# Kernel optimization log

Measured on AMD Instinct MI355X. Metric: run time of the kernel, lower is better.

Reference implementation:

```python
import jax, jax.numpy as jnp
import numpy as np

D = 1024          # dim_in == dim_out
H = 16            # num_heads
G = 4             # num_kv_groups
HD = D // H       # head_dim = 64
GS = H // G       # group_size = 4
S = 2048          # context_length / seq_len
B = 2
EPS = 1e-05


def setup_inputs() -> dict:
    key = jax.random.key(0)
    ks = jax.random.split(key, 12)
    sd = 0.02
    return {
        "x":  jax.random.normal(ks[0], (B, S, D), jnp.float32),
        # torch.nn.Linear weights are stored [out_features, in_features]
        "wq": jax.random.normal(ks[1], (D, D), jnp.float32) * sd,
        "wk": jax.random.normal(ks[2], (G * HD, D), jnp.float32) * sd,
        "wv": jax.random.normal(ks[3], (G * HD, D), jnp.float32) * sd,
        "wo": jax.random.normal(ks[4], (D, D), jnp.float32) * sd,
        "w1": jax.random.normal(ks[5], (4 * D, D), jnp.float32) * sd,
        "w2": jax.random.normal(ks[6], (D, 4 * D), jnp.float32) * sd,
        "g1": jnp.ones((D,), jnp.float32),
        "b1": jnp.zeros((D,), jnp.float32),
        "g2": jnp.ones((D,), jnp.float32),
        "b2": jnp.zeros((D,), jnp.float32),
    }


def _layernorm(x, gamma, beta):
    mean = jnp.mean(x, axis=-1, keepdims=True)
    var = jnp.var(x, axis=-1, keepdims=True)  # unbiased=False
    return (x - mean) * jax.lax.rsqrt(var + EPS) * gamma + beta


def _gelu_tanh(x):
    c = jnp.sqrt(jnp.asarray(2.0 / jnp.pi, x.dtype))
    return 0.5 * x * (1.0 + jnp.tanh(c * (x + 0.044715 * x ** 3)))


def _gqa(x, wq, wk, wv, wo):
    b, s, _ = x.shape
    q = (x @ wq.T).reshape(b, s, H, HD).transpose(0, 2, 1, 3)   # [B,H,S,hd]
    k = (x @ wk.T).reshape(b, s, G, HD).transpose(0, 2, 1, 3)   # [B,G,S,hd]
    v = (x @ wv.T).reshape(b, s, G, HD).transpose(0, 2, 1, 3)
    k = jnp.repeat(k, GS, axis=1)                               # [B,H,S,hd]
    v = jnp.repeat(v, GS, axis=1)
    scores = jnp.einsum('bhqd,bhkd->bhqk', q, k)                # [B,H,S,S]
    causal = jnp.tril(jnp.ones((s, s), bool))
    scores = jnp.where(causal, scores, -jnp.inf)
    attn = jax.nn.softmax(scores / jnp.sqrt(jnp.asarray(HD, scores.dtype)), axis=-1)
    ctx = jnp.einsum('bhqk,bhkd->bhqd', attn, v)                # [B,H,S,hd]
    ctx = ctx.transpose(0, 2, 1, 3).reshape(b, s, D)
    return ctx @ wo.T


def reference(x, wq, wk, wv, wo, w1, w2, g1, b1, g2, b2):
    h = x + _gqa(_layernorm(x, g1, b1), wq, wk, wv, wo)
    ff = _layernorm(h, g2, b2) @ w1.T
    ff = _gelu_tanh(ff) @ w2.T
    return h + ff
```

## Files before the change

kernel.cpp:

```cpp
#include <hip/hip_runtime.h>
#include <stdint.h>

typedef __bf16 bf16_t;
typedef bf16_t bf16x8 __attribute__((ext_vector_type(8)));
typedef bf16_t bf16x4 __attribute__((ext_vector_type(4)));
typedef float f32x4 __attribute__((ext_vector_type(4)));

#define DEVFN static __device__ __forceinline__

DEVFN void gload_lds16(const void* g, void* l) {
  __builtin_amdgcn_global_load_lds((const __attribute__((address_space(1))) void*)g,
                                   (__attribute__((address_space(3))) void*)l, 16, 0, 0);
}

DEVFN float gelu_f(float x) {
  float u = 0.7978845608028654f * (x + 0.044715f * x * x * x);
  float e = __expf(2.0f * u);
  float t = 1.0f - 2.0f / (e + 1.0f);
  return 0.5f * x * (1.0f + t);
}

template <int CTRL>
DEVFN float dpp_rot(float x) {
  int i = __builtin_bit_cast(int, x);
  int r = __builtin_amdgcn_update_dpp(i, i, CTRL, 0xF, 0xF, false);
  return __builtin_bit_cast(float, r);
}
DEVFN float dpp_sum16(float x) {
  x += dpp_rot<0x121>(x);
  x += dpp_rot<0x122>(x);
  x += dpp_rot<0x124>(x);
  x += dpp_rot<0x128>(x);
  return x;
}

__global__ void cvt_kernel(const float* __restrict__ s, bf16_t* __restrict__ d, int n4) {
  int i = blockIdx.x * blockDim.x + threadIdx.x;
  int stride = gridDim.x * blockDim.x;
  for (; i < n4; i += stride) {
    float4 v = ((const float4*)s)[i];
    bf16x4 o;
    o[0] = (bf16_t)v.x; o[1] = (bf16_t)v.y; o[2] = (bf16_t)v.z; o[3] = (bf16_t)v.w;
    ((bf16x4*)d)[i] = o;
  }
}

__global__ void cvt4_kernel(const float* __restrict__ wq, const float* __restrict__ wk,
                            const float* __restrict__ wv, const float* __restrict__ wo,
                            bf16_t* __restrict__ qkv_dst, bf16_t* __restrict__ wo_dst) {
  int i = blockIdx.x * blockDim.x + threadIdx.x;
  int stride = gridDim.x * blockDim.x;
  for (; i < 655360; i += stride) {
    const float* s;
    bf16_t* d;
    int j;
    if (i < 262144) { s = wq; d = qkv_dst; j = i; }
    else if (i < 327680) { s = wk; d = qkv_dst + 1048576; j = i - 262144; }
    else if (i < 393216) { s = wv; d = qkv_dst + 1310720; j = i - 327680; }
    else { s = wo; d = wo_dst; j = i - 393216; }
    float4 v = ((const float4*)s)[j];
    bf16x4 o;
    o[0] = (bf16_t)v.x; o[1] = (bf16_t)v.y; o[2] = (bf16_t)v.z; o[3] = (bf16_t)v.w;
    ((bf16x4*)d)[j] = o;
  }
}

__global__ __launch_bounds__(256) void ln_kernel(const float* __restrict__ in,
                                                 const float* __restrict__ gamma,
                                                 const float* __restrict__ beta,
                                                 bf16_t* __restrict__ out) {
  const int row = blockIdx.x;
  const int tid = threadIdx.x;
  const float4 v = ((const float4*)(in + (size_t)row * 1024))[tid];
  float s = v.x + v.y + v.z + v.w;
  float q = v.x * v.x + v.y * v.y + v.z * v.z + v.w * v.w;
#pragma unroll
  for (int off = 1; off < 64; off <<= 1) {
    s += __shfl_xor(s, off);
    q += __shfl_xor(q, off);
  }
  __shared__ float ss[4], qs[4];
  if ((tid & 63) == 0) { ss[tid >> 6] = s; qs[tid >> 6] = q; }
  __syncthreads();
  s = ss[0] + ss[1] + ss[2] + ss[3];
  q = qs[0] + qs[1] + qs[2] + qs[3];
  const float mean = s * (1.0f / 1024.0f);
  const float var = q * (1.0f / 1024.0f) - mean * mean;
  const float rstd = rsqrtf(var + 1e-5f);
  const float4 g4 = ((const float4*)gamma)[tid];
  const float4 b4 = ((const float4*)beta)[tid];
  bf16x4 o;
  o[0] = (bf16_t)((v.x - mean) * rstd * g4.x + b4.x);
  o[1] = (bf16_t)((v.y - mean) * rstd * g4.y + b4.y);
  o[2] = (bf16_t)((v.z - mean) * rstd * g4.z + b4.z);
  o[3] = (bf16_t)((v.w - mean) * rstd * g4.w + b4.w);
  *(bf16x4*)(out + (size_t)row * 1024 + tid * 4) = o;
}

template <int EPI>
__global__ __launch_bounds__(256, 3)
void gemm_bt(const bf16_t* __restrict__ A, const bf16_t* __restrict__ W,
             bf16_t* outb, float* outf, const float* resid, int M, int N, int K) {
  __shared__ __align__(16) bf16_t As[4][64 * 32];
  __shared__ __align__(16) bf16_t Bs[4][128 * 32];
  const int tid = threadIdx.x;
  const int lane = tid & 63;
  const int wid = tid >> 6;
  const int l15 = lane & 15;
  const int l4 = lane >> 4;

  const int nwg = gridDim.x * gridDim.y;
  const int bid = blockIdx.y * gridDim.x + blockIdx.x;
  const int cpx = nwg >> 3;
  const int swz = (bid & 7) * cpx + (bid >> 3);
  const int m0 = (swz / gridDim.x) * 64;
  const int n0 = (swz % gridDim.x) * 128;

  const int wr = wid >> 1;
  const int wc = wid & 1;

  const int sr = lane >> 2;
  const int sk = (lane & 3) * 8;
  const bf16_t* aBase = A + (size_t)(m0 + wid * 16 + sr) * K + sk;
  const bf16_t* bBase = W + (size_t)(n0 + wid * 32 + sr) * K + sk;
  const size_t rowOff16 = (size_t)16 * K;

  f32x4 acc[2][4] = {};
  const int NT = K / 32;

  auto stage = [&](int buf, int t) {
    const int ko = t * 32;
    gload_lds16(aBase + ko, &As[buf][wid * 512]);
    gload_lds16(bBase + ko, &Bs[buf][wid * 1024]);
    gload_lds16(bBase + ko + rowOff16, &Bs[buf][wid * 1024 + 512]);
  };

  stage(0, 0);
  if (NT > 1) stage(1, 1);
  if (NT > 2) stage(2, 2);

  for (int t = 0; t < NT; ++t) {
    if (t + 2 < NT)      __builtin_amdgcn_s_waitcnt(0xF76);
    else if (t + 1 < NT) __builtin_amdgcn_s_waitcnt(0xF73);
    else                 __builtin_amdgcn_s_waitcnt(0xF70);
    __builtin_amdgcn_s_barrier();
    __builtin_amdgcn_sched_barrier(0);
    if (t + 3 < NT) stage((t + 3) & 3, t + 3);
    const int buf = t & 3;
    bf16x8 af[2], bfr[4];
#pragma unroll
    for (int i = 0; i < 2; ++i)
      af[i] = *(const bf16x8*)&As[buf][(wr * 32 + i * 16 + l15) * 32 + l4 * 8];
#pragma unroll
    for (int j = 0; j < 4; ++j)
      bfr[j] = *(const bf16x8*)&Bs[buf][(wc * 64 + j * 16 + l15) * 32 + l4 * 8];
#pragma unroll
    for (int i = 0; i < 2; ++i)
#pragma unroll
      for (int j = 0; j < 4; ++j)
        acc[i][j] = __builtin_amdgcn_mfma_f32_16x16x32_bf16(af[i], bfr[j], acc[i][j], 0, 0, 0);
  }

  const int col0 = n0 + wc * 64 + l15;
  const int row0 = m0 + wr * 32 + l4 * 4;
#pragma unroll
  for (int i = 0; i < 2; ++i) {
#pragma unroll
    for (int r = 0; r < 4; ++r) {
      const size_t row = (size_t)(row0 + i * 16 + r);
#pragma unroll
      for (int j = 0; j < 4; ++j) {
        const size_t idx = row * N + col0 + j * 16;
        const float v = acc[i][j][r];
        if constexpr (EPI == 0) {
          outb[idx] = (bf16_t)v;
        } else if constexpr (EPI == 1) {
          outb[idx] = (bf16_t)gelu_f(v);
        } else {
          outf[idx] = resid[idx] + v;
        }
      }
    }
  }
}

static __device__ const int kQbTab[40] = {0,1,2,3,4,4,5,5,6,6,7,7,8,8,8,9,9,9,10,10,10,
                                          11,11,11,12,12,12,12,13,13,13,13,14,14,14,14,15,15,15,15};
static __device__ const int kCTab[40]  = {0,0,0,0,0,1,0,1,0,1,0,1,0,1,2,0,1,2,0,1,2,
                                          0,1,2,0,1,2,3,0,1,2,3,0,1,2,3,0,1,2,3};
static __device__ const int kPrefix16[16] = {0,1,2,3,4,6,8,10,12,15,18,21,24,28,32,36};

__global__ __launch_bounds__(256, 3) void attn_kernel(const bf16_t* __restrict__ qkv,
                                                      bf16_t* __restrict__ pO,
                                                      float* __restrict__ pML) {
  __shared__ __align__(16) bf16_t Ks[2][64 * 68];
  __shared__ __align__(16) bf16_t Vt[2][64 * 68];
  __shared__ __align__(16) bf16_t Ps[4][32 * 68];
  const int tid = threadIdx.x, lane = tid & 63, wid = tid >> 6;
  const int l15 = lane & 15, l4 = lane >> 4;
  const int bx = blockIdx.x;
  const int qb = kQbTab[bx] * 128;
  const int kv_lo = kCTab[bx] * 512;
  const int kv_hi = min(qb + 128, kv_lo + 512);
  const int h = blockIdx.y, b = blockIdx.z;
  const int g = h >> 2;
  const int slot = (b * 16 + h) * 40 + bx;
  const size_t RS = 1536;
  const bf16_t* qbase = qkv + (size_t)b * 2048 * RS + h * 64;
  const bf16_t* kbase = qkv + (size_t)b * 2048 * RS + 1024 + g * 64;
  const bf16_t* vbase = kbase + 256;
  const float C2S = 0.125f * 1.44269504088896340736f;

  bf16x8 qf[2][2];
#pragma unroll
  for (int rf = 0; rf < 2; ++rf)
#pragma unroll
    for (int kc = 0; kc < 2; ++kc) {
      bf16x8 raw = *(const bf16x8*)(qbase + (size_t)(qb + wid * 32 + rf * 16 + l15) * RS +
                                    kc * 32 + l4 * 8);
#pragma unroll
      for (int e = 0; e < 8; ++e) qf[rf][kc][e] = (bf16_t)((float)raw[e] * C2S);
    }

  f32x4 po[2][4] = {};
  float l_i[2][4] = {};

  const int sKrow = tid >> 2, sKc = (tid & 3) * 16;
  const int sVkey = tid & 63, sVd = (tid >> 6) * 16;
  const bf16_t* kRowPtr = kbase + (size_t)sKrow * RS + sKc;
  const bf16_t* vRowPtr = vbase + (size_t)sVkey * RS + sVd;

  uint4 k0 = *(const uint4*)(kRowPtr + (size_t)kv_lo * RS);
  uint4 k1 = *(const uint4*)(kRowPtr + (size_t)kv_lo * RS + 8);
  bf16x8 v0 = *(const bf16x8*)(vRowPtr + (size_t)kv_lo * RS);
  bf16x8 v1 = *(const bf16x8*)(vRowPtr + (size_t)kv_lo * RS + 8);
  *(uint4*)&Ks[0][sKrow * 68 + sKc] = k0;
  *(uint4*)&Ks[0][sKrow * 68 + sKc + 8] = k1;
#pragma unroll
  for (int i = 0; i < 8; ++i) {
    Vt[0][(sVd + i) * 68 + sVkey] = v0[i];
    Vt[0][(sVd + 8 + i) * 68 + sVkey] = v1[i];
  }

  const int fb0 = qb + wid * 32;
  int cur = 0;
  for (int kv0 = kv_lo; kv0 < kv_hi; kv0 += 64) {
    __syncthreads();
    const bool more = (kv0 + 64) < kv_hi;
    if (more) {
      const bf16_t* kp = kRowPtr + (size_t)(kv0 + 64) * RS;
      const bf16_t* vp = vRowPtr + (size_t)(kv0 + 64) * RS;
      k0 = *(const uint4*)kp;
      k1 = *(const uint4*)(kp + 8);
      v0 = *(const bf16x8*)vp;
      v1 = *(const bf16x8*)(vp + 8);
    }

    f32x4 sAcc[2][4] = {};
#pragma unroll
    for (int jt = 0; jt < 4; ++jt) {
#pragma unroll
      for (int kc = 0; kc < 2; ++kc) {
        bf16x8 kf = *(const bf16x8*)&Ks[cur][(jt * 16 + l15) * 68 + kc * 32 + l4 * 8];
        sAcc[0][jt] = __builtin_amdgcn_mfma_f32_16x16x32_bf16(qf[0][kc], kf, sAcc[0][jt], 0, 0, 0);
        sAcc[1][jt] = __builtin_amdgcn_mfma_f32_16x16x32_bf16(qf[1][kc], kf, sAcc[1][jt], 0, 0, 0);
      }
    }

#pragma unroll
    for (int rf = 0; rf < 2; ++rf) {
      const int fb = fb0 + rf * 16;
      if (kv0 > fb + 15) continue;
      bf16_t* psb = &Ps[wid][(rf * 16 + l4 * 4) * 68 + l15];
      float rsum[4] = {0.f, 0.f, 0.f, 0.f};
      const bool diag = (kv0 + 63 > fb);
#pragma unroll
      for (int jt = 0; jt < 4; ++jt)
#pragma unroll
        for (int r = 0; r < 4; ++r) {
          float sv = sAcc[rf][jt][r];
          if (diag) {
            const int key = kv0 + jt * 16 + l15;
            sv = (key <= fb + l4 * 4 + r) ? sv : -3.0e38f;
          }
          const float e = exp2f(sv);
          rsum[r] += e;
          psb[r * 68 + jt * 16] = (bf16_t)e;
        }
#pragma unroll
      for (int r = 0; r < 4; ++r) l_i[rf][r] += dpp_sum16(rsum[r]);
    }

    if (kv0 <= fb0 + 31) {
      const bool do0 = (kv0 <= fb0 + 15);
#pragma unroll
      for (int kc = 0; kc < 2; ++kc) {
        bf16x8 pa1 = *(const bf16x8*)&Ps[wid][(16 + l15) * 68 + kc * 32 + l4 * 8];
        bf16x8 pa0;
        if (do0) pa0 = *(const bf16x8*)&Ps[wid][l15 * 68 + kc * 32 + l4 * 8];
#pragma unroll
        for (int jd = 0; jd < 4; ++jd) {
          bf16x8 vf = *(const bf16x8*)&Vt[cur][(jd * 16 + l15) * 68 + kc * 32 + l4 * 8];
          if (do0) po[0][jd] = __builtin_amdgcn_mfma_f32_16x16x32_bf16(pa0, vf, po[0][jd], 0, 0, 0);
          po[1][jd] = __builtin_amdgcn_mfma_f32_16x16x32_bf16(pa1, vf, po[1][jd], 0, 0, 0);
        }
      }
    }

    if (more) {
      *(uint4*)&Ks[cur ^ 1][sKrow * 68 + sKc] = k0;
      *(uint4*)&Ks[cur ^ 1][sKrow * 68 + sKc + 8] = k1;
#pragma unroll
      for (int i = 0; i < 8; ++i) {
        Vt[cur ^ 1][(sVd + i) * 68 + sVkey] = v0[i];
        Vt[cur ^ 1][(sVd + 8 + i) * 68 + sVkey] = v1[i];
      }
    }
    cur ^= 1;
  }

#pragma unroll
  for (int rf = 0; rf < 2; ++rf) {
#pragma unroll
    for (int r = 0; r < 4; ++r) {
      const int lrow = wid * 32 + rf * 16 + l4 * 4 + r;
      if (l15 == 0) {
        pML[((size_t)slot * 128 + lrow) * 2] = 0.0f;
        pML[((size_t)slot * 128 + lrow) * 2 + 1] = l_i[rf][r];
      }
#pragma unroll
      for (int jd = 0; jd < 4; ++jd)
        pO[((size_t)slot * 128 + lrow) * 64 + jd * 16 + l15] = (bf16_t)po[rf][jd][r];
    }
  }
}

__global__ __launch_bounds__(256) void attn_combine(const bf16_t* __restrict__ pO,
                                                    const float* __restrict__ pML,
                                                    bf16_t* __restrict__ ctx) {
  const int i = blockIdx.x, h = blockIdx.y, b = blockIdx.z;
  const int C = (i >> 2) + 1;
  const int base = (b * 16 + h) * 40 + kPrefix16[i];
  const int row = threadIdx.x >> 1;
  const int half = (threadIdx.x & 1) * 32;
  float m = -3.0e38f;
  for (int c = 0; c < C; ++c)
    m = fmaxf(m, pML[((size_t)(base + c) * 128 + row) * 2]);
  float L = 0.0f, acc[32];
#pragma unroll
  for (int e = 0; e < 32; ++e) acc[e] = 0.0f;
  for (int c = 0; c < C; ++c) {
    const float mc = pML[((size_t)(base + c) * 128 + row) * 2];
    const float lc = pML[((size_t)(base + c) * 128 + row) * 2 + 1];
    const float w = exp2f(mc - m);
    L += w * lc;
    const bf16_t* op = pO + ((size_t)(base + c) * 128 + row) * 64 + half;
#pragma unroll
    for (int j = 0; j < 4; ++j) {
      bf16x8 v = *(const bf16x8*)(op + j * 8);
#pragma unroll
      for (int e = 0; e < 8; ++e) acc[j * 8 + e] += w * (float)v[e];
    }
  }
  const float inv = 1.0f / L;
  bf16_t* outp = ctx + ((size_t)b * 2048 + i * 128 + row) * 1024 + h * 64 + half;
#pragma unroll
  for (int j = 0; j < 4; ++j) {
    bf16x8 o;
#pragma unroll
    for (int e = 0; e < 8; ++e) o[e] = (bf16_t)(acc[j * 8 + e] * inv);
    *(bf16x8*)(outp + j * 8) = o;
  }
}

extern "C" void kernel_launch(void* const* d_in, const int* in_sizes, int n_in,
                              void* d_out, int out_size, void* d_ws, size_t ws_size,
                              hipStream_t stream) {
  const float* x = (const float*)d_in[0];
  const float* wq = (const float*)d_in[1];
  const float* wk = (const float*)d_in[2];
  const float* wv = (const float*)d_in[3];
  const float* wo = (const float*)d_in[4];
  const float* w1 = (const float*)d_in[5];
  const float* w2 = (const float*)d_in[6];
  const float* g1 = (const float*)d_in[7];
  const float* b1 = (const float*)d_in[8];
  const float* g2 = (const float*)d_in[9];
  const float* b2 = (const float*)d_in[10];
  float* out = (float*)d_out;

  char* ws = (char*)d_ws;
  bf16_t* qkv = (bf16_t*)(ws + 0);
  bf16_t* ctx = (bf16_t*)(ws + 12582912);
  bf16_t* wo_b = (bf16_t*)(ws + 20971520);
  bf16_t* wqkv_b = (bf16_t*)(ws + 23068672);
  bf16_t* h1 = (bf16_t*)(ws + 26214400);
  bf16_t* pO = (bf16_t*)(ws + 23068672);
  float* pML = (float*)(ws + 45088768);
  bf16_t* w1_b = (bf16_t*)(ws + 0);
  bf16_t* w2_b = (bf16_t*)(ws + 8388608);
  bf16_t* h2 = (bf16_t*)(ws + 16777216);
  bf16_t* ff = (bf16_t*)(ws + 25165824);

  auto cvt = [&](const float* s, bf16_t* d, int n) {
    int n4 = n / 4;
    int grid = (n4 + 255) / 256;
    if (grid > 2048) grid = 2048;
    cvt_kernel<<<grid, 256, 0, stream>>>(s, d, n4);
  };
  cvt4_kernel<<<2048, 256, 0, stream>>>(wq, wk, wv, wo, wqkv_b, wo_b);

  ln_kernel<<<4096, 256, 0, stream>>>(x, g1, b1, h1);
  gemm_bt<0><<<dim3(12, 64), 256, 0, stream>>>(h1, wqkv_b, qkv, nullptr, nullptr, 4096, 1536, 1024);
  attn_kernel<<<dim3(40, 16, 2), 256, 0, stream>>>(qkv, pO, pML);
  cvt(w1, w1_b, 4194304);
  attn_combine<<<dim3(16, 16, 2), 256, 0, stream>>>(pO, pML, ctx);
  gemm_bt<2><<<dim3(8, 64), 256, 0, stream>>>(ctx, wo_b, nullptr, out, x, 4096, 1024, 1024);
  cvt(w2, w2_b, 4194304);
  ln_kernel<<<4096, 256, 0, stream>>>(out, g2, b2, h2);
  gemm_bt<1><<<dim3(32, 64), 256, 0, stream>>>(h2, w1_b, ff, nullptr, nullptr, 4096, 4096, 1024);
  gemm_bt<2><<<dim3(8, 64), 256, 0, stream>>>(ff, w2_b, nullptr, out, out, 4096, 1024, 4096);
}
```

Measured before the change: 283.1 us.

## Replace GEMM with 128x128x64 tile, 8-wave kernel using XOR-swizzled LDS

The bf16 GEMM kernel is rebuilt around 128x128 output tiles with a K-step of 64 and 512 threads (8 waves, each computing 64x32). LDS columns are XOR-swizzled to avoid bank conflicts, and s_setprio is raised around the MFMA block. The larger tiles raise arithmetic intensity and cut global traffic per FLOP. In exchange the kernel uses 128KB of LDS per block and launches fewer workgroups, which may hurt occupancy and load balance on the smaller N=1024 GEMMs.

```diff
diff --git a/kernel.cpp b/kernel.cpp
--- a/kernel.cpp
+++ b/kernel.cpp
@@ -98,80 +98,100 @@
 }
 
 template <int EPI>
-__global__ __launch_bounds__(256, 3)
-void gemm_bt(const bf16_t* __restrict__ A, const bf16_t* __restrict__ W,
-             bf16_t* outb, float* outf, const float* resid, int M, int N, int K) {
-  __shared__ __align__(16) bf16_t As[4][64 * 32];
-  __shared__ __align__(16) bf16_t Bs[4][128 * 32];
+__global__ __launch_bounds__(512, 2)
+void gemm8(const bf16_t* __restrict__ A, const bf16_t* __restrict__ W,
+           bf16_t* outb, float* outf, const float* resid, int M, int N, int K) {
+  __shared__ __align__(16) bf16_t As[4][8192];
+  __shared__ __align__(16) bf16_t Bs[4][8192];
   const int tid = threadIdx.x;
   const int lane = tid & 63;
   const int wid = tid >> 6;
   const int l15 = lane & 15;
   const int l4 = lane >> 4;
-
-  const int nwg = gridDim.x * gridDim.y;
-  const int bid = blockIdx.y * gridDim.x + blockIdx.x;
+  const int wm = wid >> 2;
+  const int wn = wid & 3;
+
+  const int gx = gridDim.x;
+  const int nwg = gx * gridDim.y;
+  const int bid = blockIdx.y * gx + blockIdx.x;
   const int cpx = nwg >> 3;
   const int swz = (bid & 7) * cpx + (bid >> 3);
-  const int m0 = (swz / gridDim.x) * 64;
-  const int n0 = (swz % gridDim.x) * 128;
-
-  const int wr = wid >> 1;
-  const int wc = wid & 1;
-
-  const int sr = lane >> 2;
-  const int sk = (lane & 3) * 8;
-  const bf16_t* aBase = A + (size_t)(m0 + wid * 16 + sr) * K + sk;
-  const bf16_t* bBase = W + (size_t)(n0 + wid * 32 + sr) * K + sk;
-  const size_t rowOff16 = (size_t)16 * K;
-
-  f32x4 acc[2][4] = {};
-  const int NT = K / 32;
+  const int m0 = (swz / gx) * 128;
+  const int n0 = (swz % gx) * 128;
+
+  const int srow = tid >> 3;
+  const int scol = (((tid & 7) ^ (srow & 7)) << 3);
+  const bf16_t* aSrc = A + (size_t)(m0 + srow) * K + scol;
+  const bf16_t* bSrc = W + (size_t)(n0 + srow) * K + scol;
+  const size_t row64 = (size_t)64 * K;
 
   auto stage = [&](int buf, int t) {
-    const int ko = t * 32;
-    gload_lds16(aBase + ko, &As[buf][wid * 512]);
-    gload_lds16(bBase + ko, &Bs[buf][wid * 1024]);
-    gload_lds16(bBase + ko + rowOff16, &Bs[buf][wid * 1024 + 512]);
+    const int ko = t * 64;
+    gload_lds16(aSrc + ko,         &As[buf][wid * 512]);
+    gload_lds16(aSrc + ko + row64, &As[buf][4096 + wid * 512]);
+    gload_lds16(bSrc + ko,         &Bs[buf][wid * 512]);
+    gload_lds16(bSrc + ko + row64, &Bs[buf][4096 + wid * 512]);
   };
 
-  stage(0, 0);
-  if (NT > 1) stage(1, 1);
-  if (NT > 2) stage(2, 2);
-
+  const int g01 = l4 ^ (l15 & 7);
+  int offA[4][2], offB[2][2];
+#pragma unroll
+  for (int mf = 0; mf < 4; ++mf)
+#pragma unroll
+    for (int kk = 0; kk < 2; ++kk)
+      offA[mf][kk] = (wm * 64 + mf * 16 + l15) * 64 + ((g01 ^ (kk << 2)) << 3);
+#pragma unroll
+  for (int nf = 0; nf < 2; ++nf)
+#pragma unroll
+    for (int kk = 0; kk < 2; ++kk)
+      offB[nf][kk] = (wn * 32 + nf * 16 + l15) * 64 + ((g01 ^ (kk << 2)) << 3);
+
+  f32x4 acc[4][2] = {};
+  const int NT = K / 64;
+
+  stage(0, 0); stage(1, 1); stage(2, 2);
   for (int t = 0; t < NT; ++t) {
-    if (t + 2 < NT)      __builtin_amdgcn_s_waitcnt(0xF76);
-    else if (t + 1 < NT) __builtin_amdgcn_s_waitcnt(0xF73);
+    if (t + 2 < NT)      __builtin_amdgcn_s_waitcnt(0xF78);
+    else if (t + 1 < NT) __builtin_amdgcn_s_waitcnt(0xF74);
     else                 __builtin_amdgcn_s_waitcnt(0xF70);
     __builtin_amdgcn_s_barrier();
     __builtin_amdgcn_sched_barrier(0);
     if (t + 3 < NT) stage((t + 3) & 3, t + 3);
     const int buf = t & 3;
-    bf16x8 af[2], bfr[4];
-#pragma unroll
-    for (int i = 0; i < 2; ++i)
-      af[i] = *(const bf16x8*)&As[buf][(wr * 32 + i * 16 + l15) * 32 + l4 * 8];
-#pragma unroll
-    for (int j = 0; j < 4; ++j)
-      bfr[j] = *(const bf16x8*)&Bs[buf][(wc * 64 + j * 16 + l15) * 32 + l4 * 8];
-#pragma unroll
-    for (int i = 0; i < 2; ++i)
-#pragma unroll
-      for (int j = 0; j < 4; ++j)
-        acc[i][j] = __builtin_amdgcn_mfma_f32_16x16x32_bf16(af[i], bfr[j], acc[i][j], 0, 0, 0);
-  }
-
-  const int col0 = n0 + wc * 64 + l15;
-  const int row0 = m0 + wr * 32 + l4 * 4;
-#pragma unroll
-  for (int i = 0; i < 2; ++i) {
-#pragma unroll
-    for (int r = 0; r < 4; ++r) {
-      const size_t row = (size_t)(row0 + i * 16 + r);
-#pragma unroll
-      for (int j = 0; j < 4; ++j) {
-        const size_t idx = row * N + col0 + j * 16;
-        const float v = acc[i][j][r];
+    bf16x8 af[4][2], bfr[2][2];
+#pragma unroll
+    for (int mf = 0; mf < 4; ++mf)
+#pragma unroll
+      for (int kk = 0; kk < 2; ++kk)
+        af[mf][kk] = *(const bf16x8*)&As[buf][offA[mf][kk]];
+#pragma unroll
+    for (int nf = 0; nf < 2; ++nf)
+#pragma unroll
+      for (int kk = 0; kk < 2; ++kk)
+        bfr[nf][kk] = *(const bf16x8*)&Bs[buf][offB[nf][kk]];
+    __builtin_amdgcn_s_setprio(1);
+#pragma unroll
+    for (int kk = 0; kk < 2; ++kk)
+#pragma unroll
+      for (int mf = 0; mf < 4; ++mf)
+#pragma unroll
+        for (int nf = 0; nf < 2; ++nf)
+          acc[mf][nf] = __builtin_amdgcn_mfma_f32_16x16x32_bf16(af[mf][kk], bfr[nf][kk],
+                                                                acc[mf][nf], 0, 0, 0);
+    __builtin_amdgcn_s_setprio(0);
+  }
+
+  const int col0 = n0 + wn * 32 + l15;
+  const int row0 = m0 + wm * 64 + l4 * 4;
+#pragma unroll
+  for (int mf = 0; mf < 4; ++mf) {
+#pragma unroll
+    for (int rr = 0; rr < 4; ++rr) {
+      const size_t row = (size_t)(row0 + mf * 16 + rr);
+#pragma unroll
+      for (int nf = 0; nf < 2; ++nf) {
+        const size_t idx = row * N + col0 + nf * 16;
+        const float v = acc[mf][nf][rr];
         if constexpr (EPI == 0) {
           outb[idx] = (bf16_t)v;
         } else if constexpr (EPI == 1) {
@@ -411,13 +431,13 @@
   cvt4_kernel<<<2048, 256, 0, stream>>>(wq, wk, wv, wo, wqkv_b, wo_b);
 
   ln_kernel<<<4096, 256, 0, stream>>>(x, g1, b1, h1);
-  gemm_bt<0><<<dim3(12, 64), 256, 0, stream>>>(h1, wqkv_b, qkv, nullptr, nullptr, 4096, 1536, 1024);
+  gemm8<0><<<dim3(12, 32), 512, 0, stream>>>(h1, wqkv_b, qkv, nullptr, nullptr, 4096, 1536, 1024);
   attn_kernel<<<dim3(40, 16, 2), 256, 0, stream>>>(qkv, pO, pML);
   cvt(w1, w1_b, 4194304);
   attn_combine<<<dim3(16, 16, 2), 256, 0, stream>>>(pO, pML, ctx);
-  gemm_bt<2><<<dim3(8, 64), 256, 0, stream>>>(ctx, wo_b, nullptr, out, x, 4096, 1024, 1024);
+  gemm8<2><<<dim3(8, 32), 512, 0, stream>>>(ctx, wo_b, nullptr, out, x, 4096, 1024, 1024);
   cvt(w2, w2_b, 4194304);
   ln_kernel<<<4096, 256, 0, stream>>>(out, g2, b2, h2);
-  gemm_bt<1><<<dim3(32, 64), 256, 0, stream>>>(h2, w1_b, ff, nullptr, nullptr, 4096, 4096, 1024);
-  gemm_bt<2><<<dim3(8, 64), 256, 0, stream>>>(ff, w2_b, nullptr, out, out, 4096, 1024, 4096);
-}
+  gemm8<1><<<dim3(32, 32), 512, 0, stream>>>(h2, w1_b, ff, nullptr, nullptr, 4096, 4096, 1024);
+  gemm8<2><<<dim3(8, 32), 512, 0, stream>>>(ff, w2_b, nullptr, out, out, 4096, 1024, 4096);
+}
```

After: 293.6 us. 1.04x slower.
